# Performance work log

Measured on AMD Instinct MI355X. Metric: run time of the kernel, lower is better.

The kernel has to match this reference:

```python
import jax, jax.numpy as jnp
import numpy as np
from jax import lax

N, D = 8, 32            # batch, map_depth
S = 2                   # belief_downsample_factor
HS, WS = 512, 512       # semantic map resolution
H, W = HS // S, WS // S # belief resolution (256, 256)
K = 7                   # motion_kernel_size
KK = K * K
HID = 64                # motion_hidden_size
A = 256                 # action_embedding_size


def _conv(x, w, b, pad, dil=1):
    # x: NCHW, w: OIHW
    y = lax.conv_general_dilated(
        x, w, window_strides=(1, 1), padding=[(pad, pad), (pad, pad)],
        rhs_dilation=(dil, dil), dimension_numbers=('NCHW', 'OIHW', 'NCHW'))
    return y + b[None, :, None, None]


def _unfold_index():
    # Reproduces nn.Unfold([K,K]) applied to ConstantPad2d(K//2, -1)(arange image).
    # Result flattened in (ki*K+kj, i, j) order, matching col2im flatten order.
    pad = K // 2
    img = np.arange(H * W, dtype=np.int64).reshape(H, W)
    imgp = np.pad(img, ((pad, pad), (pad, pad)), constant_values=-1)
    idx = np.empty((K, K, H, W), dtype=np.int64)
    for ki in range(K):
        for kj in range(K):
            idx[ki, kj] = imgp[ki:ki + H, kj:kj + W]
    return idx.reshape(-1)  # (K*K*H*W,)

_IDX = _unfold_index()
_VALID = _IDX >= 0
_IDX_SAFE = np.where(_VALID, _IDX, 0)


def _scatter_logsumexp(src, idx, num_segments):
    # src: (B, M) with -inf marking invalid entries; idx: (M,) shared across B.
    def one(s):
        mx = jax.ops.segment_max(s, idx, num_segments=num_segments)          # (P,)
        g = mx[idx]                                                          # (M,)
        contrib = jnp.where(jnp.isneginf(s), 0.0,
                            jnp.exp(s - jnp.where(jnp.isfinite(g), g, 0.0)))
        sm = jax.ops.segment_sum(contrib, idx, num_segments=num_segments)    # (P,)
        return mx + jnp.log(jnp.where(jnp.isfinite(mx), sm, 1.0))
    return jax.vmap(one)(src)


def setup_inputs() -> dict:
    key = jax.random.key(0)
    ks = jax.random.split(key, 20)
    f32 = jnp.float32
    return {
        'log_belief': jax.random.normal(ks[0], (N, 1, H, W), f32),
        'semantic_map': jax.random.normal(ks[1], (N, D, HS, WS), f32),
        'action': jax.random.normal(ks[2], (N, A), f32),
        # Bottleneck(map_depth -> hidden -> map_depth, dilations [3,1])
        'w_in': jax.random.normal(ks[3], (HID, D, 1, 1), f32) * 0.1,
        'b_in': jnp.zeros((HID,), f32),
        'w_d3': jax.random.normal(ks[4], (HID, HID, 3, 3), f32) * 0.05,
        'b_d3': jnp.zeros((HID,), f32),
        'w_d1': jax.random.normal(ks[5], (HID, HID, 3, 3), f32) * 0.05,
        'b_d1': jnp.zeros((HID,), f32),
        'w_out': jax.random.normal(ks[6], (D, HID, 1, 1), f32) * 0.1,
        'b_out': jnp.zeros((D,), f32),
        # conv1x1: map_depth -> K*K
        'w_k': jax.random.normal(ks[7], (KK, D, 1, 1), f32) * 0.1,
        'b_k': jnp.zeros((KK,), f32),
        # DenseMlpBlock2: A -> hidden -> K*K
        'w_a1': jax.random.normal(ks[8], (A, HID), f32) * 0.05,
        'b_a1': jnp.zeros((HID,), f32),
        'w_a2': jax.random.normal(ks[9], (HID, KK), f32) * 0.05,
        'b_a2': jnp.zeros((KK,), f32),
    }


def reference(log_belief, semantic_map, action,
              w_in, b_in, w_d3, b_d3, w_d1, b_d1, w_out, b_out,
              w_k, b_k, w_a1, b_a1, w_a2, b_a2):
    # Dropout in eval mode -> identity. MaxPool2d(S, stride=S):
    x = lax.reduce_window(semantic_map, -jnp.inf, lax.max,
                          (1, 1, S, S), (1, 1, S, S), 'VALID')  # (N,D,H,W)
    # Bottleneck (conv1x1 -> dilated 3x3 convs -> conv1x1, residual)
    h = jax.nn.relu(_conv(x, w_in, b_in, 0))
    h = jax.nn.relu(_conv(h, w_d3, b_d3, 3, 3))
    h = jax.nn.relu(_conv(h, w_d1, b_d1, 1, 1))
    x2 = x + _conv(h, w_out, b_out, 0)
    # motion kernel logits over K*K taps per pixel
    motion = jax.nn.log_softmax(_conv(x2, w_k, b_k, 0), axis=1)   # (N,KK,H,W)
    lang = jax.nn.log_softmax(
        jax.nn.relu(action @ w_a1 + b_a1) @ w_a2 + b_a2, axis=1)  # (N,KK)
    log_kernel = jax.nn.log_softmax(motion + lang[:, :, None, None], axis=1)
    # propagate_belief: col2im + scatter_logsumexp (C=1, Cin=Cout=1)
    src = (log_belief + log_kernel).reshape(N, -1)                # (N, KK*H*W)
    idx = jnp.asarray(_IDX_SAFE)
    src = jnp.where(jnp.asarray(_VALID)[None, :], src, -jnp.inf)
    new_belief = _scatter_logsumexp(src, idx, H * W)              # (N, H*W)
    return new_belief.reshape(N, 1, H, W)
```

## Files before the change

kernel.cpp:

```cpp
#include <hip/hip_runtime.h>
#include <hip/hip_bf16.h>

typedef __hip_bfloat16 bf16;
typedef __attribute__((ext_vector_type(8)))  short  short8;
typedef __attribute__((ext_vector_type(16))) float  floatx16;

#define HW 65536

__device__ __forceinline__ float b2f(bf16 v){ return __bfloat162float(v); }
__device__ __forceinline__ bf16  f2b(float v){ return __float2bfloat16(v); }
__device__ __forceinline__ unsigned short f2bu(float v){
  union { bf16 h; unsigned short u; } cv; cv.h = __float2bfloat16(v); return cv.u;
}
__device__ __forceinline__ float bu2f(unsigned short u){
  union { unsigned u; float f; } cv; cv.u = ((unsigned)u) << 16; return cv.f;
}

__global__ __launch_bounds__(256) void setup_kernel(
    const float* __restrict__ w_d3, const float* __restrict__ w_d1,
    bf16* __restrict__ wb3, bf16* __restrict__ wb1,
    const float* __restrict__ action,
    const float* __restrict__ w_a1, const float* __restrict__ b_a1,
    const float* __restrict__ w_a2, const float* __restrict__ b_a2,
    float* __restrict__ lang){
  int b = blockIdx.x;
  if (b < 288){
    const float* w = (b < 144) ? w_d3 : w_d1;
    bf16* wb = (b < 144) ? wb3 : wb1;
    int i = (b < 144 ? b : b - 144)*256 + threadIdx.x;
    if (i >= 36864) return;
    int j    = i & 7;
    int gran = i >> 3;
    int oc   = gran & 63;
    int rest = gran >> 6;
    int half = rest & 1;
    int ks   = (rest >> 1) & 3;
    int t    = rest >> 3;
    int e  = ks*16 + half*8 + j;
    int ki = t / 3, kj = t - ki*3;
    wb[i] = f2b(w[(oc*64 + e)*9 + ki*3 + kj]);
  } else {
    int n = b - 288;
    int t = threadIdx.x;
    __shared__ float part[256];
    __shared__ float hid[64];
    int d = t & 63, q = t >> 6;
    const float* ar = action + n*256;
    float a = 0.f;
    #pragma unroll 8
    for (int i = q*64; i < q*64 + 64; i++) a += ar[i]*w_a1[i*64 + d];
    part[t] = a;
    __syncthreads();
    if (t < 64)
      hid[t] = fmaxf(b_a1[t] + part[t] + part[64+t] + part[128+t] + part[192+t], 0.f);
    __syncthreads();
    if (t < 49){
      float l = b_a2[t];
      #pragma unroll 8
      for (int j2 = 0; j2 < 64; j2++) l += hid[j2]*w_a2[j2*49 + t];
      lang[n*49 + t] = l;
    }
  }
}

__global__ __launch_bounds__(256) void pool_in_kernel(
    const float* __restrict__ sm, const float* __restrict__ w_in,
    const float* __restrict__ b_in, float* __restrict__ x, bf16* __restrict__ h1){
  int p = blockIdx.x*256 + threadIdx.x;
  int n = p >> 16; int ij = p & 65535; int i = ij >> 8; int j = ij & 255;
  const float* smn = sm + ((long)n << 23);
  float xv[32];
  #pragma unroll
  for (int d = 0; d < 32; d++){
    long base = ((long)(d*512 + 2*i) << 9) + 2*j;
    float2 p0 = *reinterpret_cast<const float2*>(smn + base);
    float2 p1 = *reinterpret_cast<const float2*>(smn + base + 512);
    xv[d] = fmaxf(fmaxf(p0.x, p0.y), fmaxf(p1.x, p1.y));
  }
  float4* xo = reinterpret_cast<float4*>(x + ((long)p << 5));
  #pragma unroll
  for (int q = 0; q < 8; q++)
    xo[q] = make_float4(xv[4*q], xv[4*q+1], xv[4*q+2], xv[4*q+3]);
  unsigned ow[32];
  #pragma unroll 4
  for (int c = 0; c < 64; c += 2){
    float a0 = b_in[c], a1 = b_in[c+1];
    #pragma unroll
    for (int d = 0; d < 32; d++){
      a0 += xv[d]*w_in[c*32+d];
      a1 += xv[d]*w_in[(c+1)*32+d];
    }
    ow[c>>1] = ((unsigned)f2bu(fmaxf(a1,0.f)) << 16) | f2bu(fmaxf(a0,0.f));
  }
  uint4* ho = reinterpret_cast<uint4*>((char*)h1 + ((long)p << 7));
  #pragma unroll
  for (int q = 0; q < 8; q++)
    ho[q] = make_uint4(ow[4*q], ow[4*q+1], ow[4*q+2], ow[4*q+3]);
}

template<int DIL>
__global__ __launch_bounds__(256) void conv3x3_mfma(
    const bf16* __restrict__ hin, const bf16* __restrict__ wb,
    const float* __restrict__ bias, bf16* __restrict__ hout){
  constexpr int R = 16 + 2*DIL, C = 16 + 2*DIL, NPIX = R*C;
  __shared__ __align__(16) char tile[NPIX*128];
  int b = blockIdx.x;
  int n = b >> 8; int tb = b & 255;
  int i0 = (tb >> 4) << 4, j0 = (tb & 15) << 4;
  int tid = threadIdx.x;
  const bf16* hn = hin + ((long)n << 22);
  for (int s = tid; s < NPIX*8; s += 256){
    int pix = s >> 3, g = s & 7;
    int r = pix / C, c = pix - r*C;
    int gi = i0 - DIL + r, gj = j0 - DIL + c;
    uint4 v = make_uint4(0u,0u,0u,0u);
    if (gi >= 0 && gi < 256 && gj >= 0 && gj < 256)
      v = *reinterpret_cast<const uint4*>(hn + (((long)((gi<<8) + gj)) << 6) + (g<<3));
    *reinterpret_cast<uint4*>(tile + pix*128 + ((g ^ (pix & 7)) << 4)) = v;
  }
  __syncthreads();
  int lane = tid & 63, wv = tid >> 6;
  int l31 = lane & 31, half = lane >> 5;
  floatx16 acc[2][2];
  #pragma unroll
  for (int m2 = 0; m2 < 2; m2++){
    acc[m2][0] = (floatx16)(0.0f);
    acc[m2][1] = (floatx16)(0.0f);
  }
  int prr[2], pcc[2];
  #pragma unroll
  for (int m2 = 0; m2 < 2; m2++){
    int pidx = (wv*2 + m2)*32 + l31;
    prr[m2] = pidx >> 4; pcc[m2] = pidx & 15;
  }
  const char* wbc = reinterpret_cast<const char*>(wb);
  for (int t = 0; t < 9; t++){
    int ki = t / 3, kj = t - ki*3;
    int pp[2];
    #pragma unroll
    for (int m2 = 0; m2 < 2; m2++)
      pp[m2] = (prr[m2] + ki*DIL)*C + (pcc[m2] + kj*DIL);
    short8 bfr[4][2];
    #pragma unroll
    for (int ks = 0; ks < 4; ks++){
      #pragma unroll
      for (int nt = 0; nt < 2; nt++)
        bfr[ks][nt] = *reinterpret_cast<const short8*>(
            wbc + ((((t*4 + ks)*2 + half)*64 + nt*32 + l31) << 4));
    }
    #pragma unroll
    for (int ks = 0; ks < 4; ks++){
      #pragma unroll
      for (int m2 = 0; m2 < 2; m2++){
        short8 afrag = *reinterpret_cast<const short8*>(
            tile + pp[m2]*128 + (((ks*2 + half) ^ (pp[m2] & 7)) << 4));
        acc[m2][0] = __builtin_amdgcn_mfma_f32_32x32x16_bf16(afrag, bfr[ks][0], acc[m2][0], 0, 0, 0);
        acc[m2][1] = __builtin_amdgcn_mfma_f32_32x32x16_bf16(afrag, bfr[ks][1], acc[m2][1], 0, 0, 0);
      }
    }
  }
  float bv0 = bias[l31], bv1 = bias[32 + l31];
  bf16* ho = hout + ((long)n << 22);
  #pragma unroll
  for (int m2 = 0; m2 < 2; m2++){
    #pragma unroll
    for (int reg = 0; reg < 16; reg++){
      int row = (reg & 3) + 8*(reg >> 2) + 4*half;
      int pidx = (wv*2 + m2)*32 + row;
      int pr = pidx >> 4, pc = pidx & 15;
      long off = ((long)(((i0+pr)<<8) + (j0+pc))) << 6;
      ho[off + l31]      = f2b(fmaxf(acc[m2][0][reg] + bv0, 0.f));
      ho[off + 32 + l31] = f2b(fmaxf(acc[m2][1][reg] + bv1, 0.f));
    }
  }
}

__global__ __launch_bounds__(256) void out_motion_kernel(
    const bf16* __restrict__ h3, const float* __restrict__ x,
    const float* __restrict__ w_out, const float* __restrict__ b_out,
    const float* __restrict__ w_k, const float* __restrict__ b_k,
    const float* __restrict__ lang, float* __restrict__ lk){
  int p = blockIdx.x*256 + threadIdx.x;
  int n = p >> 16; int ij = p & 65535;
  float hv[64];
  const uint4* hp = reinterpret_cast<const uint4*>((const char*)h3 + ((long)p << 7));
  #pragma unroll
  for (int q = 0; q < 8; q++){
    uint4 u = hp[q];
    unsigned uu[4] = {u.x, u.y, u.z, u.w};
    #pragma unroll
    for (int k = 0; k < 4; k++){
      hv[q*8 + 2*k]   = bu2f((unsigned short)(uu[k] & 0xffffu));
      hv[q*8 + 2*k+1] = bu2f((unsigned short)(uu[k] >> 16));
    }
  }
  float o[32];
  const float4* xp = reinterpret_cast<const float4*>(x + ((long)p << 5));
  #pragma unroll
  for (int q = 0; q < 8; q++){
    float4 tq = xp[q];
    o[4*q] = tq.x; o[4*q+1] = tq.y; o[4*q+2] = tq.z; o[4*q+3] = tq.w;
  }
  #pragma unroll 4
  for (int d = 0; d < 32; d++){
    float acc = b_out[d];
    #pragma unroll
    for (int e = 0; e < 64; e++) acc += hv[e]*w_out[d*64+e];
    o[d] += acc;
  }
  float lg[49]; float m = -1e30f;
  #pragma unroll 7
  for (int k = 0; k < 49; k++){
    float acc = b_k[k] + lang[n*49+k];
    #pragma unroll
    for (int d = 0; d < 32; d++) acc += o[d]*w_k[k*32+d];
    lg[k] = acc; m = fmaxf(m, acc);
  }
  float s = 0.f;
  #pragma unroll
  for (int k = 0; k < 49; k++) s += __expf(lg[k]-m);
  float lse = m + __logf(s);
  #pragma unroll
  for (int k = 0; k < 49; k++) lk[(long)n*49*HW + (long)k*HW + ij] = lg[k] - lse;
}

__global__ __launch_bounds__(256) void gather_lse_kernel(
    const float* __restrict__ lb, const float* __restrict__ lk, float* __restrict__ out){
  int p = blockIdx.x*256 + threadIdx.x;
  int n = p >> 16; int ij = p & 65535; int i = ij >> 8; int j = ij & 255;
  const float* lkn = lk + (long)n*49*HW;
  float v[49]; float m = -1e30f;
  #pragma unroll
  for (int ki = 0; ki < 7; ki++){
    int h = i + 3 - ki;
    bool hok = (h >= 0 && h < 256);
    #pragma unroll
    for (int kj = 0; kj < 7; kj++){
      int w = j + 3 - kj;
      float val = -1e30f;
      if (hok && w >= 0 && w < 256){
        int q = h*256 + w;
        val = lb[n*HW + q] + lkn[(ki*7+kj)*HW + q];
      }
      v[ki*7+kj] = val; m = fmaxf(m, val);
    }
  }
  float s = 0.f;
  #pragma unroll
  for (int t = 0; t < 49; t++) s += __expf(v[t]-m);
  out[p] = m + __logf(s);
}

extern "C" void kernel_launch(void* const* d_in, const int* in_sizes, int n_in,
                              void* d_out, int out_size, void* d_ws, size_t ws_size,
                              hipStream_t stream) {
  (void)in_sizes; (void)n_in; (void)out_size; (void)ws_size;
  const float* lb    = (const float*)d_in[0];
  const float* sm    = (const float*)d_in[1];
  const float* act   = (const float*)d_in[2];
  const float* w_in  = (const float*)d_in[3];
  const float* b_in  = (const float*)d_in[4];
  const float* w_d3  = (const float*)d_in[5];
  const float* b_d3  = (const float*)d_in[6];
  const float* w_d1  = (const float*)d_in[7];
  const float* b_d1  = (const float*)d_in[8];
  const float* w_out = (const float*)d_in[9];
  const float* b_out = (const float*)d_in[10];
  const float* w_k   = (const float*)d_in[11];
  const float* b_k   = (const float*)d_in[12];
  const float* w_a1  = (const float*)d_in[13];
  const float* b_a1  = (const float*)d_in[14];
  const float* w_a2  = (const float*)d_in[15];
  const float* b_a2  = (const float*)d_in[16];
  float* out = (float*)d_out;

  char* ws = (char*)d_ws;
  float* x    = (float*)(ws + 0);
  bf16*  h1   = (bf16*) (ws + 67108864);
  bf16*  h2   = (bf16*) (ws + 134217728);
  float* lk   = (float*)(ws + 134217728);
  float* lang = (float*)(ws + 236978176);
  bf16*  wb3  = (bf16*) (ws + 236979968);
  bf16*  wb1  = (bf16*) (ws + 237053696);

  setup_kernel<<<296, 256, 0, stream>>>(w_d3, w_d1, wb3, wb1,
                                        act, w_a1, b_a1, w_a2, b_a2, lang);
  pool_in_kernel<<<2048, 256, 0, stream>>>(sm, w_in, b_in, x, h1);
  conv3x3_mfma<3><<<2048, 256, 0, stream>>>(h1, wb3, b_d3, h2);
  conv3x3_mfma<1><<<2048, 256, 0, stream>>>(h2, wb1, b_d1, h1);
  out_motion_kernel<<<2048, 256, 0, stream>>>(h1, x, w_out, b_out,
                                              w_k, b_k, lang, lk);
  gather_lse_kernel<<<2048, 256, 0, stream>>>(lb, lk, out);
}
```

Before: 694.2 us.

## Store pooled features and log-kernel in fp16, interleave batch in block order

The pooled input x and the 49-tap log-kernel intermediate are now stored as fp16 instead of fp32, halving their write and read traffic between kernels. The conv and gather kernels also remap block indices so consecutive blocks cover different batch images at the same spatial tile. The goal is to cut memory bandwidth on the large intermediates, at the cost of reduced precision in the residual path and the log-kernel values.

```diff
diff --git a/kernel.cpp b/kernel.cpp
--- a/kernel.cpp
+++ b/kernel.cpp
@@ -2,6 +2,7 @@
 #include <hip/hip_bf16.h>
 
 typedef __hip_bfloat16 bf16;
+typedef _Float16 fp16;
 typedef __attribute__((ext_vector_type(8)))  short  short8;
 typedef __attribute__((ext_vector_type(16))) float  floatx16;
 
@@ -14,6 +15,12 @@
 }
 __device__ __forceinline__ float bu2f(unsigned short u){
   union { unsigned u; float f; } cv; cv.u = ((unsigned)u) << 16; return cv.f;
+}
+__device__ __forceinline__ unsigned short f2hu(float v){
+  union { fp16 h; unsigned short u; } cv; cv.h = (fp16)v; return cv.u;
+}
+__device__ __forceinline__ float hu2f(unsigned short u){
+  union { fp16 h; unsigned short u; } cv; cv.u = u; return (float)cv.h;
 }
 
 __global__ __launch_bounds__(256) void setup_kernel(
@@ -65,7 +72,7 @@
 
 __global__ __launch_bounds__(256) void pool_in_kernel(
     const float* __restrict__ sm, const float* __restrict__ w_in,
-    const float* __restrict__ b_in, float* __restrict__ x, bf16* __restrict__ h1){
+    const float* __restrict__ b_in, fp16* __restrict__ x, bf16* __restrict__ h1){
   int p = blockIdx.x*256 + threadIdx.x;
   int n = p >> 16; int ij = p & 65535; int i = ij >> 8; int j = ij & 255;
   const float* smn = sm + ((long)n << 23);
@@ -77,10 +84,14 @@
     float2 p1 = *reinterpret_cast<const float2*>(smn + base + 512);
     xv[d] = fmaxf(fmaxf(p0.x, p0.y), fmaxf(p1.x, p1.y));
   }
-  float4* xo = reinterpret_cast<float4*>(x + ((long)p << 5));
-  #pragma unroll
-  for (int q = 0; q < 8; q++)
-    xo[q] = make_float4(xv[4*q], xv[4*q+1], xv[4*q+2], xv[4*q+3]);
+  unsigned xw[16];
+  #pragma unroll
+  for (int q = 0; q < 16; q++)
+    xw[q] = ((unsigned)f2hu(xv[2*q+1]) << 16) | f2hu(xv[2*q]);
+  uint4* xo = reinterpret_cast<uint4*>((char*)x + ((long)p << 6));
+  #pragma unroll
+  for (int q = 0; q < 4; q++)
+    xo[q] = make_uint4(xw[4*q], xw[4*q+1], xw[4*q+2], xw[4*q+3]);
   unsigned ow[32];
   #pragma unroll 4
   for (int c = 0; c < 64; c += 2){
@@ -105,7 +116,7 @@
   constexpr int R = 16 + 2*DIL, C = 16 + 2*DIL, NPIX = R*C;
   __shared__ __align__(16) char tile[NPIX*128];
   int b = blockIdx.x;
-  int n = b >> 8; int tb = b & 255;
+  int n = b & 7; int tb = b >> 3;
   int i0 = (tb >> 4) << 4, j0 = (tb & 15) << 4;
   int tid = threadIdx.x;
   const bf16* hn = hin + ((long)n << 22);
@@ -176,10 +187,10 @@
 }
 
 __global__ __launch_bounds__(256) void out_motion_kernel(
-    const bf16* __restrict__ h3, const float* __restrict__ x,
+    const bf16* __restrict__ h3, const fp16* __restrict__ x,
     const float* __restrict__ w_out, const float* __restrict__ b_out,
     const float* __restrict__ w_k, const float* __restrict__ b_k,
-    const float* __restrict__ lang, float* __restrict__ lk){
+    const float* __restrict__ lang, fp16* __restrict__ lk){
   int p = blockIdx.x*256 + threadIdx.x;
   int n = p >> 16; int ij = p & 65535;
   float hv[64];
@@ -195,11 +206,16 @@
     }
   }
   float o[32];
-  const float4* xp = reinterpret_cast<const float4*>(x + ((long)p << 5));
-  #pragma unroll
-  for (int q = 0; q < 8; q++){
-    float4 tq = xp[q];
-    o[4*q] = tq.x; o[4*q+1] = tq.y; o[4*q+2] = tq.z; o[4*q+3] = tq.w;
+  const uint4* xp = reinterpret_cast<const uint4*>((const char*)x + ((long)p << 6));
+  #pragma unroll
+  for (int q = 0; q < 4; q++){
+    uint4 u = xp[q];
+    unsigned uu[4] = {u.x, u.y, u.z, u.w};
+    #pragma unroll
+    for (int k = 0; k < 4; k++){
+      o[q*8 + 2*k]   = hu2f((unsigned short)(uu[k] & 0xffffu));
+      o[q*8 + 2*k+1] = hu2f((unsigned short)(uu[k] >> 16));
+    }
   }
   #pragma unroll 4
   for (int d = 0; d < 32; d++){
@@ -221,14 +237,17 @@
   for (int k = 0; k < 49; k++) s += __expf(lg[k]-m);
   float lse = m + __logf(s);
   #pragma unroll
-  for (int k = 0; k < 49; k++) lk[(long)n*49*HW + (long)k*HW + ij] = lg[k] - lse;
+  for (int k = 0; k < 49; k++)
+    lk[(long)n*49*HW + (long)k*HW + ij] = (fp16)(lg[k] - lse);
 }
 
 __global__ __launch_bounds__(256) void gather_lse_kernel(
-    const float* __restrict__ lb, const float* __restrict__ lk, float* __restrict__ out){
-  int p = blockIdx.x*256 + threadIdx.x;
-  int n = p >> 16; int ij = p & 65535; int i = ij >> 8; int j = ij & 255;
-  const float* lkn = lk + (long)n*49*HW;
+    const float* __restrict__ lb, const fp16* __restrict__ lk, float* __restrict__ out){
+  int b = blockIdx.x;
+  int n = b & 7;
+  int ij = ((b >> 3) << 8) | threadIdx.x;
+  int i = ij >> 8; int j = ij & 255;
+  const fp16* lkn = lk + (long)n*49*HW;
   float v[49]; float m = -1e30f;
   #pragma unroll
   for (int ki = 0; ki < 7; ki++){
@@ -240,7 +259,7 @@
       float val = -1e30f;
       if (hok && w >= 0 && w < 256){
         int q = h*256 + w;
-        val = lb[n*HW + q] + lkn[(ki*7+kj)*HW + q];
+        val = lb[n*HW + q] + (float)lkn[(ki*7+kj)*HW + q];
       }
       v[ki*7+kj] = val; m = fmaxf(m, val);
     }
@@ -248,7 +267,7 @@
   float s = 0.f;
   #pragma unroll
   for (int t = 0; t < 49; t++) s += __expf(v[t]-m);
-  out[p] = m + __logf(s);
+  out[n*HW + ij] = m + __logf(s);
 }
 
 extern "C" void kernel_launch(void* const* d_in, const int* in_sizes, int n_in,
@@ -275,10 +294,10 @@
   float* out = (float*)d_out;
 
   char* ws = (char*)d_ws;
-  float* x    = (float*)(ws + 0);
+  fp16*  x    = (fp16*) (ws + 0);
   bf16*  h1   = (bf16*) (ws + 67108864);
   bf16*  h2   = (bf16*) (ws + 134217728);
-  float* lk   = (float*)(ws + 134217728);
+  fp16*  lk   = (fp16*) (ws + 134217728);
   float* lang = (float*)(ws + 236978176);
   bf16*  wb3  = (bf16*) (ws + 236979968);
   bf16*  wb1  = (bf16*) (ws + 237053696);
```

Result: faster. 679.5 us (-2.1%).
